# Kernel tuning notes

Hardware: AMD Instinct MI355X
Metric: run time of the kernel (lower is better)

## Reference

```python
import jax, jax.numpy as jnp
import numpy as np

N_NODES = 100000
N_EDGES = 1600000
D = 32


def setup_inputs() -> dict:
    key = jax.random.key(0)
    k1, k2, k3, k4, k5, k6, k7 = jax.random.split(key, 7)
    x = jax.random.normal(k1, (N_NODES, D), dtype=jnp.float32)
    edge_index = jax.random.randint(k2, (2, N_EDGES), 0, N_NODES, dtype=jnp.int64)
    edge_weight = jax.random.uniform(k3, (N_EDGES,), dtype=jnp.float32)
    s = 1.0 / np.sqrt(D)
    W1 = jax.random.uniform(k4, (D, D), jnp.float32, -s, s)
    b1 = jax.random.uniform(k5, (D,), jnp.float32, -s, s)
    W2 = jax.random.uniform(k6, (D, D), jnp.float32, -s, s)
    b2 = jax.random.uniform(k7, (D,), jnp.float32, -s, s)
    return {"x": x, "edge_index": edge_index, "edge_weight": edge_weight,
            "W1": W1, "b1": b1, "W2": W2, "b2": b2}


def reference(x, edge_index, edge_weight, W1, b1, W2, b2):
    N = x.shape[0]
    src, dst = edge_index[0], edge_index[1]
    # gcn_norm with improved=True: self-loops get fill value 2.0
    loops = jnp.arange(N, dtype=edge_index.dtype)
    src_a = jnp.concatenate([src, loops])
    dst_a = jnp.concatenate([dst, loops])
    w_a = jnp.concatenate([edge_weight, jnp.full((N,), 2.0, x.dtype)])
    deg = jax.ops.segment_sum(w_a, dst_a, num_segments=N)          # [N]
    dinv = jnp.where(deg > 0, jax.lax.rsqrt(deg), 0.0)             # deg^-1/2, inf->0
    norm = dinv[src_a] * w_a * dinv[dst_a]                          # [E+N]

    def gcn_conv(h, W, b):
        h = h @ W                                                   # [N,D] dense transform
        msg = h[src_a] * norm[:, None]                              # gather + normalize [E+N,D]
        return jax.ops.segment_sum(msg, dst_a, num_segments=N) + b  # scatter-add + bias

    h = jax.nn.relu(gcn_conv(x, W1, b1))
    h = jax.nn.relu(gcn_conv(h, W2, b2))
    # F.dropout treated as identity (deterministic inference reference)
    return h
```

## Files before the change

kernel.cpp:

```cpp
#include <hip/hip_runtime.h>

#define D       32
#define BS      256
#define CBLK    500
#define CBLKP   500
#define MAXBUCK 2048
#define MAX_EPT 13
#define ECAP    4096
#define POISON_BASE ((int)0xAAAAAAAAu)

__device__ inline unsigned bf16pack2(float a, float b) {
    unsigned ua = __float_as_uint(a);
    unsigned ub = __float_as_uint(b);
    ua = (ua + 0x7FFFu + ((ua >> 16) & 1)) >> 16;
    ub = (ub + 0x7FFFu + ((ub >> 16) & 1)) >> 16;
    return ua | (ub << 16);
}
__device__ inline uint2 bf16pack4(float4 v) {
    return make_uint2(bf16pack2(v.x, v.y), bf16pack2(v.z, v.w));
}
__device__ inline float4 bf16unpack4(uint2 h) {
    return make_float4(__uint_as_float(h.x << 16),
                       __uint_as_float(h.x & 0xFFFF0000u),
                       __uint_as_float(h.y << 16),
                       __uint_as_float(h.y & 0xFFFF0000u));
}

__global__ void k_localsort_gemm(const int* __restrict__ dst, const int* __restrict__ src,
                                 const float* __restrict__ w, int* __restrict__ bc,
                                 int* __restrict__ locoff, int2* __restrict__ staged,
                                 int E, int EPB, int NBUCK, int NBUCKP,
                                 const float* __restrict__ X, const float* __restrict__ Wm,
                                 uint2* __restrict__ H, int n) {
    __shared__ int    bins[MAXBUCK];
    __shared__ int    sscan[BS];
    __shared__ int    carry;
    __shared__ float4 Ws[D * 8];
    int t = threadIdx.x;

    if ((int)blockIdx.x >= CBLK) {
        for (int i = t; i < D * 8; i += BS) Ws[i] = ((const float4*)Wm)[i];
        __syncthreads();
        int gid  = (blockIdx.x - CBLK) * BS + t;
        int node = gid >> 3;
        int q    = gid & 7;
        if (node >= n) return;
        float4 xv  = ((const float4*)X)[node * 8 + q];
        float4 acc = make_float4(0.f, 0.f, 0.f, 0.f);
#pragma unroll
        for (int k = 0; k < D; ++k) {
            float comp = (k & 3) == 0 ? xv.x : (k & 3) == 1 ? xv.y
                       : (k & 3) == 2 ? xv.z : xv.w;
            float  xk = __shfl(comp, k >> 2, 8);
            float4 wr = Ws[k * 8 + q];
            acc.x += xk * wr.x; acc.y += xk * wr.y;
            acc.z += xk * wr.z; acc.w += xk * wr.w;
        }
        H[node * 8 + q] = bf16pack4(acc);
        return;
    }

    int blk = blockIdx.x;
    int beg = blk * EPB;
    int end = min(E, beg + EPB);
    for (int i = t; i < NBUCK; i += BS) bins[i] = 0;
    __syncthreads();

    int stash[MAX_EPT];
#pragma unroll
    for (int i = 0; i < MAX_EPT; ++i) {
        int e = beg + i * BS + t;
        stash[i] = -1;
        if (e < end) {
            int dv = dst[e];
            int b  = dv >> 6;
            int r  = atomicAdd(&bins[b], 1);
            stash[i] = (b << 19) | ((dv & 63) << 13) | r;
        }
    }
    __syncthreads();
    for (int i = t; i < NBUCK; i += BS) bc[blk * NBUCKP + i] = bins[i];
    __syncthreads();
    if (t == 0) carry = 0;
    __syncthreads();
    for (int base = 0; base < NBUCK; base += BS) {
        int idx = base + t;
        int v = (idx < NBUCK) ? bins[idx] : 0;
        sscan[t] = v;
        __syncthreads();
        for (int off = 1; off < BS; off <<= 1) {
            int u = (t >= off) ? sscan[t - off] : 0;
            __syncthreads();
            sscan[t] += u;
            __syncthreads();
        }
        if (idx < NBUCK) bins[idx] = carry + sscan[t] - v;
        __syncthreads();
        if (t == 0) carry += sscan[BS - 1];
        __syncthreads();
    }
    for (int i = t; i < NBUCK; i += BS) locoff[blk * NBUCKP + i] = bins[i];
    __syncthreads();

    int2* myslice = staged + (size_t)blk * EPB;
#pragma unroll
    for (int i = 0; i < MAX_EPT; ++i) {
        if (stash[i] >= 0) {
            int e     = beg + i * BS + t;
            int b     = stash[i] >> 19;
            int local = (stash[i] >> 13) & 63;
            int r     = stash[i] & 0x1FFF;
            int pos   = bins[b] + r;
            myslice[pos] = make_int2(src[e] | (local << 17), __float_as_int(w[e]));
        }
    }
}

__global__ void k_trans(const int* __restrict__ bc, const int* __restrict__ locoff,
                        int* __restrict__ bcT, int* __restrict__ locoffT,
                        int NBUCK, int NBUCKP) {
    __shared__ int tile[32][33];
    const int* in  = (blockIdx.z == 0) ? bc  : locoff;
    int*       out = (blockIdx.z == 0) ? bcT : locoffT;
    int c0 = blockIdx.x * 32;
    int r0 = blockIdx.y * 32;
    int tx = threadIdx.x & 31, ty = threadIdx.x >> 5;
    for (int dy = ty; dy < 32; dy += 8) {
        int r = r0 + dy, c = c0 + tx;
        tile[dy][tx] = (r < CBLK && c < NBUCK) ? in[r * NBUCKP + c] : 0;
    }
    __syncthreads();
    for (int dy = ty; dy < 32; dy += 8) {
        int c = c0 + dy, r = r0 + tx;
        if (c < NBUCK && r < CBLK) out[c * CBLKP + r] = tile[tx][dy];
    }
}

__global__ void k_btot(const int* __restrict__ bcT, int* __restrict__ btot, int NBUCK) {
    int gid = blockIdx.x * BS + threadIdx.x;
    int b = gid >> 3, c = gid & 7;
    if (b >= NBUCK) return;
    int s = 0;
    for (int k = c; k < CBLK; k += 8) s += bcT[b * CBLKP + k];
    s += __shfl_xor(s, 4, 8);
    s += __shfl_xor(s, 2, 8);
    s += __shfl_xor(s, 1, 8);
    if (c == 0) btot[b] = s;
}

__global__ void k_scanB(const int* __restrict__ asum, int* __restrict__ aex, int m) {
    __shared__ int s[BS];
    __shared__ int carry;
    int t = threadIdx.x;
    if (t == 0) carry = 0;
    __syncthreads();
    for (int base = 0; base < m; base += BS) {
        int i = base + t;
        int v = (i < m) ? asum[i] : 0;
        s[t] = v;
        __syncthreads();
        for (int off = 1; off < BS; off <<= 1) {
            int u = (t >= off) ? s[t - off] : 0;
            __syncthreads();
            s[t] += u;
            __syncthreads();
        }
        if (i < m) aex[i] = carry + s[t] - v;
        __syncthreads();
        if (t == BS - 1) carry += s[BS - 1];
        __syncthreads();
    }
}

__global__ void k_merge(const int* __restrict__ bcT, const int* __restrict__ locoffT,
                        const int* __restrict__ boff, const int2* __restrict__ staged,
                        int2* __restrict__ emeta, int* __restrict__ rowptr,
                        float* __restrict__ dinv, int N, int E, int NBUCK, int EPB) {
    __shared__ int2  ebuf[ECAP];
    __shared__ int   runoff[CBLK];
    __shared__ int   lrun[CBLK];
    __shared__ int   sscan[BS];
    __shared__ int   carry;
    __shared__ int   ihist[64];
    __shared__ float fdeg[64];
    __shared__ int   cursor[64];
    int b = blockIdx.x, t = threadIdx.x;

    for (int k = t; k < CBLK; k += BS) {
        runoff[k] = bcT[b * CBLKP + k];
        lrun[k]   = locoffT[b * CBLKP + k];
    }
    if (t < 64) { ihist[t] = 0; fdeg[t] = 0.0f; }
    if (t == 0) carry = 0;
    __syncthreads();
    for (int base = 0; base < CBLK; base += BS) {
        int idx = base + t;
        int v = (idx < CBLK) ? runoff[idx] : 0;
        sscan[t] = v;
        __syncthreads();
        for (int off = 1; off < BS; off <<= 1) {
            int u = (t >= off) ? sscan[t - off] : 0;
            __syncthreads();
            sscan[t] += u;
            __syncthreads();
        }
        if (idx < CBLK) runoff[idx] = carry + sscan[t] - v;
        __syncthreads();
        if (t == 0) carry += sscan[BS - 1];
        __syncthreads();
    }
    int total  = carry;
    int bstart = boff[b];
    bool fits  = total <= ECAP;

    for (int k = t; k < CBLK; k += BS) {
        int gs = runoff[k];
        int ge = (k + 1 < CBLK) ? runoff[k + 1] : total;
        const int2* run = staged + (size_t)k * EPB + lrun[k];
        for (int j = 0; j < ge - gs; ++j) {
            int2 v = run[j];
            int local = (v.x >> 17) & 63;
            atomicAdd(&ihist[local], 1);
            atomicAdd(&fdeg[local], __int_as_float(v.y));
            if (fits) ebuf[gs + j] = v;
        }
    }
    __syncthreads();
    if (t < 64) {
        int v = ihist[t];
        int incl = v;
#pragma unroll
        for (int off = 1; off < 64; off <<= 1) {
            int u = __shfl_up(incl, off, 64);
            if (t >= off) incl += u;
        }
        int excl = incl - v;
        int node = b * 64 + t;
        if (node < N) {
            rowptr[node] = bstart + excl;
            dinv[node]   = rsqrtf(2.0f + fdeg[t]);
        }
        if (b == NBUCK - 1 && t == 0) rowptr[N] = E;
        cursor[t] = excl;
    }
    __syncthreads();
    for (int k = t; k < CBLK; k += BS) {
        int gs = runoff[k];
        int ge = (k + 1 < CBLK) ? runoff[k + 1] : total;
        const int2* run = staged + (size_t)k * EPB + lrun[k];
        for (int j = 0; j < ge - gs; ++j) {
            int2 v = fits ? ebuf[gs + j] : run[j];
            int local = (v.x >> 17) & 63;
            int r = atomicAdd(&cursor[local], 1);
            emeta[bstart + r] = make_int2(v.x & 0x1FFFF, v.y);
        }
    }
}


__global__ void k_gemm(const float* __restrict__ X, const float* __restrict__ W,
                       uint2* __restrict__ H, int n) {
    __shared__ float4 Ws[D * 8];
    int tid = threadIdx.x;
    for (int i = tid; i < D * 8; i += blockDim.x) Ws[i] = ((const float4*)W)[i];
    __syncthreads();
    int gid  = blockIdx.x * blockDim.x + tid;
    int node = gid >> 3;
    int q    = gid & 7;
    if (node >= n) return;
    float4 xv  = ((const float4*)X)[node * 8 + q];
    float4 acc = make_float4(0.f, 0.f, 0.f, 0.f);
#pragma unroll
    for (int k = 0; k < D; ++k) {
        float comp = (k & 3) == 0 ? xv.x : (k & 3) == 1 ? xv.y
                   : (k & 3) == 2 ? xv.z : xv.w;
        float  xk = __shfl(comp, k >> 2, 8);
        float4 wr = Ws[k * 8 + q];
        acc.x += xk * wr.x; acc.y += xk * wr.y;
        acc.z += xk * wr.z; acc.w += xk * wr.w;
    }
    H[node * 8 + q] = bf16pack4(acc);
}

template <bool NORM_STORE, bool FUSE_GEMM>
__global__ void k_aggregate(const int* __restrict__ rowptr, int2* __restrict__ emeta,
                            const uint2* __restrict__ H, const float* __restrict__ dinv,
                            const float* __restrict__ b, const float* __restrict__ W2,
                            void* __restrict__ outv, int n) {
    __shared__ float4 Ws[D * 8];
    int tid = threadIdx.x;
    if (FUSE_GEMM) {
        for (int i = tid; i < D * 8; i += BS) Ws[i] = ((const float4*)W2)[i];
        __syncthreads();
    }

    int gid  = blockIdx.x * BS + tid;
    int node = gid >> 3;
    int q    = gid & 7;
    if (node >= n) return;

    float  di = dinv[node];
    float  s2 = 2.0f * di * di;
    float4 bq = ((const float4*)b)[q];
    float4 h0 = bf16unpack4(H[node * 8 + q]);
    float4 acc = make_float4(h0.x * s2 + bq.x, h0.y * s2 + bq.y,
                             h0.z * s2 + bq.z, h0.w * s2 + bq.w);

    int beg  = rowptr[node];
    int end  = rowptr[node + 1];
    int full = beg + ((end - beg) & ~7);

    for (int i0 = beg; i0 < full; i0 += 8) {
        int  idx = i0 + q;
        int2 em  = emeta[idx];
        float nm;
        if (NORM_STORE) {
            nm = dinv[em.x] * __int_as_float(em.y) * di;
            emeta[idx].y = __float_as_int(nm);
        } else {
            nm = __int_as_float(em.y);
        }
#pragma unroll
        for (int j = 0; j < 8; ++j) {
            int    s   = __shfl(em.x, j, 8);
            float  nmj = __shfl(nm, j, 8);
            float4 hv  = bf16unpack4(H[s * 8 + q]);
            acc.x += nmj * hv.x; acc.y += nmj * hv.y;
            acc.z += nmj * hv.z; acc.w += nmj * hv.w;
        }
    }
    if (full < end) {
        int  idx = full + q;
        bool ok  = idx < end;
        int2 em  = ok ? emeta[idx] : make_int2(0, 0);
        float nm;
        if (NORM_STORE) {
            nm = ok ? dinv[em.x] * __int_as_float(em.y) * di : 0.0f;
            if (ok) emeta[idx].y = __float_as_int(nm);
        } else {
            nm = __int_as_float(em.y);
        }
        int rem = end - full;
        for (int j = 0; j < rem; ++j) {
            int    s   = __shfl(em.x, j, 8);
            float  nmj = __shfl(nm, j, 8);
            float4 hv  = bf16unpack4(H[s * 8 + q]);
            acc.x += nmj * hv.x; acc.y += nmj * hv.y;
            acc.z += nmj * hv.z; acc.w += nmj * hv.w;
        }
    }
    acc.x = fmaxf(acc.x, 0.f); acc.y = fmaxf(acc.y, 0.f);
    acc.z = fmaxf(acc.z, 0.f); acc.w = fmaxf(acc.w, 0.f);

    if (FUSE_GEMM) {
        float4 o = make_float4(0.f, 0.f, 0.f, 0.f);
#pragma unroll
        for (int k = 0; k < D; ++k) {
            float comp = (k & 3) == 0 ? acc.x : (k & 3) == 1 ? acc.y
                       : (k & 3) == 2 ? acc.z : acc.w;
            float  hk = __shfl(comp, k >> 2, 8);
            float4 wr = Ws[k * 8 + q];
            o.x += hk * wr.x; o.y += hk * wr.y;
            o.z += hk * wr.z; o.w += hk * wr.w;
        }
        ((uint2*)outv)[node * 8 + q] = bf16pack4(o);
    } else {
        ((float4*)outv)[node * 8 + q] = acc;
    }
}

__global__ void k_hist_gemm(const int4* __restrict__ dst4, int* __restrict__ cnt,
                            int4* __restrict__ rank4, int E4,
                            const float* __restrict__ X, const float* __restrict__ W,
                            uint2* __restrict__ H, int n, int gE4) {
    __shared__ float4 Ws[D * 8];
    int tid = threadIdx.x;
    if ((int)blockIdx.x < gE4) {
        int i = blockIdx.x * BS + tid;
        if (i >= E4) return;
        int4 d = dst4[i];
        int4 r;
        r.x = atomicAdd(&cnt[d.x], 1) - POISON_BASE;
        r.y = atomicAdd(&cnt[d.y], 1) - POISON_BASE;
        r.z = atomicAdd(&cnt[d.z], 1) - POISON_BASE;
        r.w = atomicAdd(&cnt[d.w], 1) - POISON_BASE;
        rank4[i] = r;
        return;
    }
    for (int i = tid; i < D * 8; i += BS) Ws[i] = ((const float4*)W)[i];
    __syncthreads();
    int gid  = (blockIdx.x - gE4) * BS + tid;
    int node = gid >> 3;
    int q    = gid & 7;
    if (node >= n) return;
    float4 xv  = ((const float4*)X)[node * 8 + q];
    float4 acc = make_float4(0.f, 0.f, 0.f, 0.f);
#pragma unroll
    for (int k = 0; k < D; ++k) {
        float comp = (k & 3) == 0 ? xv.x : (k & 3) == 1 ? xv.y
                   : (k & 3) == 2 ? xv.z : xv.w;
        float  xk = __shfl(comp, k >> 2, 8);
        float4 wr = Ws[k * 8 + q];
        acc.x += xk * wr.x; acc.y += xk * wr.y;
        acc.z += xk * wr.z; acc.w += xk * wr.w;
    }
    H[node * 8 + q] = bf16pack4(acc);
}

__global__ void k_scan1(const int* __restrict__ cnt, int* __restrict__ bsum, int n) {
    __shared__ int s[BS];
    int t = threadIdx.x, i = blockIdx.x * BS + t;
    s[t] = (i < n) ? (cnt[i] - POISON_BASE) : 0;
    __syncthreads();
    for (int off = BS / 2; off > 0; off >>= 1) {
        if (t < off) s[t] += s[t + off];
        __syncthreads();
    }
    if (t == 0) bsum[blockIdx.x] = s[0];
}

__global__ void k_scan23(const int* __restrict__ cnt, const int* __restrict__ bsum,
                         int* __restrict__ rowptr, int n) {
    __shared__ int red[BS];
    __shared__ int s[BS];
    int t = threadIdx.x, i = blockIdx.x * BS + t;
    int pacc = 0;
    for (int k = t; k < (int)blockIdx.x; k += BS) pacc += bsum[k];
    red[t] = pacc;
    __syncthreads();
    for (int off = BS / 2; off > 0; off >>= 1) {
        if (t < off) red[t] += red[t + off];
        __syncthreads();
    }
    int bpre = red[0];
    int v = (i < n) ? (cnt[i] - POISON_BASE) : 0;
    s[t] = v;
    __syncthreads();
    for (int off = 1; off < BS; off <<= 1) {
        int u = (t >= off) ? s[t - off] : 0;
        __syncthreads();
        s[t] += u;
        __syncthreads();
    }
    if (i < n) {
        int excl = bpre + s[t] - v;
        rowptr[i] = excl;
        if (i == n - 1) rowptr[n] = excl + v;
    }
}

__global__ void k_reorder(const int4* __restrict__ src4, const int4* __restrict__ dst4,
                          const float4* __restrict__ w4, const int4* __restrict__ rank4,
                          const int* __restrict__ rowptr, int2* __restrict__ emeta, int E4) {
    int i = blockIdx.x * blockDim.x + threadIdx.x;
    if (i >= E4) return;
    int4   s = src4[i];
    int4   d = dst4[i];
    float4 w = w4[i];
    int4   r = rank4[i];
    emeta[rowptr[d.x] + r.x] = make_int2(s.x, __float_as_int(w.x));
    emeta[rowptr[d.y] + r.y] = make_int2(s.y, __float_as_int(w.y));
    emeta[rowptr[d.z] + r.z] = make_int2(s.z, __float_as_int(w.z));
    emeta[rowptr[d.w] + r.w] = make_int2(s.w, __float_as_int(w.w));
}

__global__ void k_degF(const int* __restrict__ rowptr, const int2* __restrict__ emeta,
                       float* __restrict__ dinv, int n) {
    int gid  = blockIdx.x * blockDim.x + threadIdx.x;
    int node = gid >> 3;
    int c    = gid & 7;
    if (node >= n) return;
    int beg = rowptr[node], end = rowptr[node + 1];
    float sum = 0.0f;
    for (int idx = beg + c; idx < end; idx += 8)
        sum += __int_as_float(emeta[idx].y);
    sum += __shfl_xor(sum, 4, 8);
    sum += __shfl_xor(sum, 2, 8);
    sum += __shfl_xor(sum, 1, 8);
    if (c == 0) dinv[node] = rsqrtf(2.0f + sum);
}

extern "C" void kernel_launch(void* const* d_in, const int* in_sizes, int n_in,
                              void* d_out, int out_size, void* d_ws, size_t ws_size,
                              hipStream_t stream) {
    const float* x   = (const float*)d_in[0];
    const int*   ei  = (const int*)d_in[1];
    const float* w   = (const float*)d_in[2];
    const float* W1  = (const float*)d_in[3];
    const float* b1  = (const float*)d_in[4];
    const float* W2  = (const float*)d_in[5];
    const float* b2  = (const float*)d_in[6];
    float*       out = (float*)d_out;

    const int N = in_sizes[0] / D;
    const int E = in_sizes[2];
    const int* src = ei;
    const int* dst = ei + E;

    const int NBUCK  = (N + 63) / 64;
    const int NBUCKP = (NBUCK + 3) & ~3;
    const int EPB    = (E + CBLK - 1) / CBLK;
    const int NB     = (N + BS - 1) / BS;
    const int E4     = E / 4;
    const int gE4    = (E4 + BS - 1) / BS;
    const int gN8    = (N * 8 + BS - 1) / BS;

    char*  base    = (char*)d_ws;
    int2*  emeta   = (int2*)base;
    uint2* ht      = (uint2*)(base + (size_t)E * 8);
    uint2* ht2     = ht + (size_t)N * 8;
    float* dinv    = (float*)(ht2 + (size_t)N * 8);
    int*   rowptr  = (int*)(dinv + N);
    int2*  staged  = (int2*)(rowptr + ((N + 4) & ~3));
    int*   bc      = (int*)(staged + E);
    int*   locoff  = bc + (size_t)CBLK * NBUCKP;
    int*   bcT     = locoff + (size_t)CBLK * NBUCKP;
    int*   locoffT = bcT + (size_t)NBUCK * CBLKP;
    int*   btot    = locoffT + (size_t)NBUCK * CBLKP;
    int*   boff    = btot + NBUCKP;
    size_t need    = (size_t)((char*)(boff + NBUCKP) - base);

    bool main_ok = (ws_size >= need) && (NBUCK <= MAXBUCK) && (N < (1 << 17)) &&
                   ((EPB + BS - 1) / BS <= MAX_EPT) && (EPB <= 8192) && (N % 4 == 0);

    if (main_ok) {
        k_localsort_gemm<<<CBLK + gN8, BS, 0, stream>>>(dst, src, w, bc, locoff, staged,
                                                        E, EPB, NBUCK, NBUCKP, x, W1, ht, N);
        dim3 tg((NBUCK + 31) / 32, (CBLK + 31) / 32, 2);
        k_trans<<<tg, BS, 0, stream>>>(bc, locoff, bcT, locoffT, NBUCK, NBUCKP);
        k_btot <<<(NBUCK * 8 + BS - 1) / BS, BS, 0, stream>>>(bcT, btot, NBUCK);
        k_scanB<<<1, BS, 0, stream>>>(btot, boff, NBUCK);
        k_merge<<<NBUCK, BS, 0, stream>>>(bcT, locoffT, boff, staged, emeta, rowptr, dinv,
                                          N, E, NBUCK, EPB);
        k_aggregate<true,  true ><<<gN8, BS, 0, stream>>>(rowptr, emeta, ht,  dinv, b1, W2, ht2, N);
        k_aggregate<false, false><<<gN8, BS, 0, stream>>>(rowptr, emeta, ht2, dinv, b2, nullptr, out, N);
    } else {
        int* cnt  = (int*)staged;
        int* rank = cnt + N;
        int* bsum = rank + E;
        k_hist_gemm<<<gE4 + gN8, BS, 0, stream>>>((const int4*)dst, cnt, (int4*)rank, E4,
                                                  x, W1, ht, N, gE4);
        k_scan1 <<<NB, BS, 0, stream>>>(cnt, bsum, N);
        k_scan23<<<NB, BS, 0, stream>>>(cnt, bsum, rowptr, N);
        k_reorder<<<(E4 + BS - 1) / BS, BS, 0, stream>>>((const int4*)src, (const int4*)dst,
                                                         (const float4*)w, (const int4*)rank,
                                                         rowptr, emeta, E4);
        k_degF<<<gN8, BS, 0, stream>>>(rowptr, emeta, dinv, N);
        k_aggregate<true,  false><<<gN8, BS, 0, stream>>>(rowptr, emeta, ht, dinv, b1, nullptr, out, N);
        k_gemm<<<gN8, BS, 0, stream>>>(out, W2, ht, N);
        k_aggregate<false, false><<<gN8, BS, 0, stream>>>(rowptr, emeta, ht2, dinv, b2, nullptr, out, N);
    }
}
```

Measured before the change: 222.6 us.

## Fold symmetric normalization into pre-scaled features instead of per-edge norm

Instead of computing and storing dinv[src]*w*dinv[dst] per edge in the first aggregation, the transformed features are pre-scaled by dinv of the source node. The merge kernel does this scaling in place, and the destination dinv is applied once per node after accumulation, along with bias and ReLU. The fused GEMM output is scaled by dinv before being stored for layer two. This removes a random dinv gather and an emeta write-back per edge. The cost is an extra read-modify-write pass over H and an extra bf16 rounding of the scaled features.

```diff
diff --git a/kernel.cpp b/kernel.cpp
--- a/kernel.cpp
+++ b/kernel.cpp
@@ -175,7 +175,8 @@
 __global__ void k_merge(const int* __restrict__ bcT, const int* __restrict__ locoffT,
                         const int* __restrict__ boff, const int2* __restrict__ staged,
                         int2* __restrict__ emeta, int* __restrict__ rowptr,
-                        float* __restrict__ dinv, int N, int E, int NBUCK, int EPB) {
+                        float* __restrict__ dinv, uint2* __restrict__ H,
+                        int N, int E, int NBUCK, int EPB) {
     __shared__ int2  ebuf[ECAP];
     __shared__ int   runoff[CBLK];
     __shared__ int   lrun[CBLK];
@@ -184,6 +185,7 @@
     __shared__ int   ihist[64];
     __shared__ float fdeg[64];
     __shared__ int   cursor[64];
+    __shared__ float sdinv[64];
     int b = blockIdx.x, t = threadIdx.x;
 
     for (int k = t; k < CBLK; k += BS) {
@@ -236,12 +238,29 @@
         }
         int excl = incl - v;
         int node = b * 64 + t;
+        float di = rsqrtf(2.0f + fdeg[t]);
         if (node < N) {
             rowptr[node] = bstart + excl;
-            dinv[node]   = rsqrtf(2.0f + fdeg[t]);
-        }
+            dinv[node]   = di;
+        }
+        sdinv[t] = di;
         if (b == NBUCK - 1 && t == 0) rowptr[N] = E;
         cursor[t] = excl;
+    }
+    __syncthreads();
+    {
+        int base_node = b * 64;
+        for (int i = t; i < 64 * 8; i += BS) {
+            int row  = i >> 3;
+            int node = base_node + row;
+            if (node < N) {
+                float di = sdinv[row];
+                size_t off = (size_t)node * 8 + (i & 7);
+                float4 f = bf16unpack4(H[off]);
+                f.x *= di; f.y *= di; f.z *= di; f.w *= di;
+                H[off] = bf16pack4(f);
+            }
+        }
     }
     __syncthreads();
     for (int k = t; k < CBLK; k += BS) {
@@ -257,36 +276,11 @@
     }
 }
 
-
-__global__ void k_gemm(const float* __restrict__ X, const float* __restrict__ W,
-                       uint2* __restrict__ H, int n) {
-    __shared__ float4 Ws[D * 8];
-    int tid = threadIdx.x;
-    for (int i = tid; i < D * 8; i += blockDim.x) Ws[i] = ((const float4*)W)[i];
-    __syncthreads();
-    int gid  = blockIdx.x * blockDim.x + tid;
-    int node = gid >> 3;
-    int q    = gid & 7;
-    if (node >= n) return;
-    float4 xv  = ((const float4*)X)[node * 8 + q];
-    float4 acc = make_float4(0.f, 0.f, 0.f, 0.f);
-#pragma unroll
-    for (int k = 0; k < D; ++k) {
-        float comp = (k & 3) == 0 ? xv.x : (k & 3) == 1 ? xv.y
-                   : (k & 3) == 2 ? xv.z : xv.w;
-        float  xk = __shfl(comp, k >> 2, 8);
-        float4 wr = Ws[k * 8 + q];
-        acc.x += xk * wr.x; acc.y += xk * wr.y;
-        acc.z += xk * wr.z; acc.w += xk * wr.w;
-    }
-    H[node * 8 + q] = bf16pack4(acc);
-}
-
-template <bool NORM_STORE, bool FUSE_GEMM>
-__global__ void k_aggregate(const int* __restrict__ rowptr, int2* __restrict__ emeta,
-                            const uint2* __restrict__ H, const float* __restrict__ dinv,
-                            const float* __restrict__ b, const float* __restrict__ W2,
-                            void* __restrict__ outv, int n) {
+template <bool FUSE_GEMM>
+__global__ void k_agg(const int* __restrict__ rowptr, const int2* __restrict__ emeta,
+                      const uint2* __restrict__ Hs, const float* __restrict__ dinv,
+                      const float* __restrict__ b, const float* __restrict__ W2,
+                      void* __restrict__ outv, int n) {
     __shared__ float4 Ws[D * 8];
     int tid = threadIdx.x;
     if (FUSE_GEMM) {
@@ -300,57 +294,43 @@
     if (node >= n) return;
 
     float  di = dinv[node];
-    float  s2 = 2.0f * di * di;
     float4 bq = ((const float4*)b)[q];
-    float4 h0 = bf16unpack4(H[node * 8 + q]);
-    float4 acc = make_float4(h0.x * s2 + bq.x, h0.y * s2 + bq.y,
-                             h0.z * s2 + bq.z, h0.w * s2 + bq.w);
+    float4 h0 = bf16unpack4(Hs[node * 8 + q]);
+    float4 acc = make_float4(2.0f * h0.x, 2.0f * h0.y, 2.0f * h0.z, 2.0f * h0.w);
 
     int beg  = rowptr[node];
     int end  = rowptr[node + 1];
     int full = beg + ((end - beg) & ~7);
 
     for (int i0 = beg; i0 < full; i0 += 8) {
-        int  idx = i0 + q;
-        int2 em  = emeta[idx];
-        float nm;
-        if (NORM_STORE) {
-            nm = dinv[em.x] * __int_as_float(em.y) * di;
-            emeta[idx].y = __float_as_int(nm);
-        } else {
-            nm = __int_as_float(em.y);
-        }
+        int2 em = emeta[i0 + q];
+        float nm = __int_as_float(em.y);
 #pragma unroll
         for (int j = 0; j < 8; ++j) {
             int    s   = __shfl(em.x, j, 8);
             float  nmj = __shfl(nm, j, 8);
-            float4 hv  = bf16unpack4(H[s * 8 + q]);
+            float4 hv  = bf16unpack4(Hs[s * 8 + q]);
             acc.x += nmj * hv.x; acc.y += nmj * hv.y;
             acc.z += nmj * hv.z; acc.w += nmj * hv.w;
         }
     }
     if (full < end) {
         int  idx = full + q;
-        bool ok  = idx < end;
-        int2 em  = ok ? emeta[idx] : make_int2(0, 0);
-        float nm;
-        if (NORM_STORE) {
-            nm = ok ? dinv[em.x] * __int_as_float(em.y) * di : 0.0f;
-            if (ok) emeta[idx].y = __float_as_int(nm);
-        } else {
-            nm = __int_as_float(em.y);
-        }
+        int2 em  = (idx < end) ? emeta[idx] : make_int2(0, 0);
+        float nm = (idx < end) ? __int_as_float(em.y) : 0.0f;
         int rem = end - full;
         for (int j = 0; j < rem; ++j) {
             int    s   = __shfl(em.x, j, 8);
             float  nmj = __shfl(nm, j, 8);
-            float4 hv  = bf16unpack4(H[s * 8 + q]);
+            float4 hv  = bf16unpack4(Hs[s * 8 + q]);
             acc.x += nmj * hv.x; acc.y += nmj * hv.y;
             acc.z += nmj * hv.z; acc.w += nmj * hv.w;
         }
     }
-    acc.x = fmaxf(acc.x, 0.f); acc.y = fmaxf(acc.y, 0.f);
-    acc.z = fmaxf(acc.z, 0.f); acc.w = fmaxf(acc.w, 0.f);
+    acc.x = fmaxf(di * acc.x + bq.x, 0.f);
+    acc.y = fmaxf(di * acc.y + bq.y, 0.f);
+    acc.z = fmaxf(di * acc.z + bq.z, 0.f);
+    acc.w = fmaxf(di * acc.w + bq.w, 0.f);
 
     if (FUSE_GEMM) {
         float4 o = make_float4(0.f, 0.f, 0.f, 0.f);
@@ -363,6 +343,7 @@
             o.x += hk * wr.x; o.y += hk * wr.y;
             o.z += hk * wr.z; o.w += hk * wr.w;
         }
+        o.x *= di; o.y *= di; o.z *= di; o.w *= di;
         ((uint2*)outv)[node * 8 + q] = bf16pack4(o);
     } else {
         ((float4*)outv)[node * 8 + q] = acc;
@@ -464,8 +445,8 @@
     emeta[rowptr[d.w] + r.w] = make_int2(s.w, __float_as_int(w.w));
 }
 
-__global__ void k_degF(const int* __restrict__ rowptr, const int2* __restrict__ emeta,
-                       float* __restrict__ dinv, int n) {
+__global__ void k_degscaleF(const int* __restrict__ rowptr, const int2* __restrict__ emeta,
+                            float* __restrict__ dinv, uint2* __restrict__ H, int n) {
     int gid  = blockIdx.x * blockDim.x + threadIdx.x;
     int node = gid >> 3;
     int c    = gid & 7;
@@ -477,7 +458,13 @@
     sum += __shfl_xor(sum, 4, 8);
     sum += __shfl_xor(sum, 2, 8);
     sum += __shfl_xor(sum, 1, 8);
-    if (c == 0) dinv[node] = rsqrtf(2.0f + sum);
+    float di = rsqrtf(2.0f + sum);
+    if (c == 0) dinv[node] = di;
+    di = __shfl(di, 0, 8);
+    size_t off = (size_t)node * 8 + c;
+    float4 f = bf16unpack4(H[off]);
+    f.x *= di; f.y *= di; f.z *= di; f.w *= di;
+    H[off] = bf16pack4(f);
 }
 
 extern "C" void kernel_launch(void* const* d_in, const int* in_sizes, int n_in,
@@ -531,9 +518,9 @@
         k_btot <<<(NBUCK * 8 + BS - 1) / BS, BS, 0, stream>>>(bcT, btot, NBUCK);
         k_scanB<<<1, BS, 0, stream>>>(btot, boff, NBUCK);
         k_merge<<<NBUCK, BS, 0, stream>>>(bcT, locoffT, boff, staged, emeta, rowptr, dinv,
-                                          N, E, NBUCK, EPB);
-        k_aggregate<true,  true ><<<gN8, BS, 0, stream>>>(rowptr, emeta, ht,  dinv, b1, W2, ht2, N);
-        k_aggregate<false, false><<<gN8, BS, 0, stream>>>(rowptr, emeta, ht2, dinv, b2, nullptr, out, N);
+                                          ht, N, E, NBUCK, EPB);
+        k_agg<true ><<<gN8, BS, 0, stream>>>(rowptr, emeta, ht,  dinv, b1, W2, ht2, N);
+        k_agg<false><<<gN8, BS, 0, stream>>>(rowptr, emeta, ht2, dinv, b2, nullptr, out, N);
     } else {
         int* cnt  = (int*)staged;
         int* rank = cnt + N;
@@ -545,9 +532,8 @@
         k_reorder<<<(E4 + BS - 1) / BS, BS, 0, stream>>>((const int4*)src, (const int4*)dst,
                                                          (const float4*)w, (const int4*)rank,
                                                          rowptr, emeta, E4);
-        k_degF<<<gN8, BS, 0, stream>>>(rowptr, emeta, dinv, N);
-        k_aggregate<true,  false><<<gN8, BS, 0, stream>>>(rowptr, emeta, ht, dinv, b1, nullptr, out, N);
-        k_gemm<<<gN8, BS, 0, stream>>>(out, W2, ht, N);
-        k_aggregate<false, false><<<gN8, BS, 0, stream>>>(rowptr, emeta, ht2, dinv, b2, nullptr, out, N);
-    }
-}
+        k_degscaleF<<<gN8, BS, 0, stream>>>(rowptr, emeta, dinv, ht, N);
+        k_agg<true ><<<gN8, BS, 0, stream>>>(rowptr, emeta, ht,  dinv, b1, W2, ht2, N);
+        k_agg<false><<<gN8, BS, 0, stream>>>(rowptr, emeta, ht2, dinv, b2, nullptr, out, N);
+    }
+}
```

After: 221.9 us. Within noise of the previous version (-0.3%).
